# Kernel tuning notes

Hardware: AMD Instinct MI355X
Metric: run time of the kernel (lower is better)

Reference implementation:

```python
import jax, jax.numpy as jnp
import numpy as np

MAX_LEN = 3

def _attention(h, enc, w1, b1, w2):
    # h: [B,H], enc: [B,S,H]
    B, S, H = enc.shape
    hs = jnp.broadcast_to(h[:, None, :], (B, S, H))
    x = jnp.tanh(jnp.concatenate([enc, hs], axis=-1) @ w1.T + b1)  # [B,S,H]
    e = (x @ w2.T)[..., 0]                                         # [B,S]
    alpha = jax.nn.softmax(e, axis=1)
    return jnp.einsum('bs,bsd->bd', alpha, enc)                    # [B,H]

def _gru_cell(x, h, w_ih, w_hh, b_ih, b_hh):
    # torch GRU gate order: r, z, n
    H = h.shape[-1]
    gi = x @ w_ih.T + b_ih   # [B,3H]
    gh = h @ w_hh.T + b_hh
    i_r, i_z, i_n = gi[:, :H], gi[:, H:2*H], gi[:, 2*H:]
    h_r, h_z, h_n = gh[:, :H], gh[:, H:2*H], gh[:, 2*H:]
    r = jax.nn.sigmoid(i_r + h_r)
    z = jax.nn.sigmoid(i_z + h_z)
    n = jnp.tanh(i_n + r * h_n)
    return (1.0 - z) * n + z * h

def setup_inputs() -> dict:
    key = jax.random.key(0)
    ks = jax.random.split(key, 16)
    B, S, H, DW = 1024, 40, 1024, 512
    V0 = V1 = 4000
    EMB_N = V0 + V1 + 1
    sc = lambda fan: 1.0 / np.sqrt(fan)
    inp = {
        'encoder_outputs': jax.random.normal(ks[0], (B, S, H), jnp.float32),
        'encoder_hidden': jax.random.normal(ks[1], (1, B, H), jnp.float32),
        'targets': jax.random.randint(ks[2], (MAX_LEN, B), 0, V0),
        'emb': jax.random.normal(ks[3], (EMB_N, DW), jnp.float32) * 0.02,
        'attn_w1': jax.random.normal(ks[4], (H, 2 * H), jnp.float32) * sc(2 * H),
        'attn_b1': jnp.zeros((H,), jnp.float32),
        'attn_w2': jax.random.normal(ks[5], (1, H), jnp.float32) * sc(H),
        'w_ih': jax.random.normal(ks[6], (3 * H, H + DW), jnp.float32) * sc(H),
        'w_hh': jax.random.normal(ks[7], (3 * H, H), jnp.float32) * sc(H),
        'b_ih': jnp.zeros((3 * H,), jnp.float32),
        'b_hh': jnp.zeros((3 * H,), jnp.float32),
        'out0_w': jax.random.normal(ks[8], (V0, H), jnp.float32) * sc(H),
        'out0_b': jnp.zeros((V0,), jnp.float32),
        'out1_w': jax.random.normal(ks[9], (V1, H), jnp.float32) * sc(H),
        'out1_b': jnp.zeros((V1,), jnp.float32),
    }
    return inp

def reference(encoder_outputs, encoder_hidden, targets, emb, attn_w1, attn_b1,
              attn_w2, w_ih, w_hh, b_ih, b_hh, out0_w, out0_b, out1_w, out1_b):
    B = encoder_outputs.shape[0]
    h = encoder_hidden[0]  # n_layers=1, unidirectional -> init state passthrough
    logs = []
    for t in range(MAX_LEN):
        context = _attention(h, encoder_outputs, attn_w1, attn_b1, attn_w2)
        if t == 0:
            it = jnp.zeros((B,), jnp.int32)
        elif t == 1:
            it = targets[0] + 1
        else:
            it = targets[t - 1] + 36
        x = jnp.concatenate([emb[it], context], axis=1)  # [B, DW+H]
        h = _gru_cell(x, h, w_ih, w_hh, b_ih, b_hh)
        if t == 0 or t == 2:
            logits = h @ out0_w.T + out0_b
        else:
            logits = h @ out1_w.T + out1_b
        logs.append(jax.nn.log_softmax(logits, axis=1))
    return jnp.stack(logs)  # [MAX_LEN, B, V]
```

## Files before the change

kernel.cpp:

```cpp
#include <hip/hip_runtime.h>
#include <hip/hip_bf16.h>
#include <math.h>

#define B_SZ 1024
#define S_SZ 40
#define H_SZ 1024
#define DW_SZ 512
#define V_SZ 4000
#define XW (DW_SZ + H_SZ)
#define NGL 8192

typedef __bf16 bf16x8 __attribute__((ext_vector_type(8)));
typedef float f32x4 __attribute__((ext_vector_type(4)));

__device__ __forceinline__ float fast_tanh(float x) {
    return 1.0f - 2.0f / (1.0f + __expf(2.0f * x));
}
__device__ __forceinline__ float fast_sigmoid(float x) {
    return 1.0f / (1.0f + __expf(-x));
}
__device__ __forceinline__ float bfraw2f(unsigned short u) {
    return __uint_as_float(((unsigned)u) << 16);
}
__device__ __forceinline__ ushort4 cvt4(float4 v) {
    union { ushort4 u; __hip_bfloat16 h[4]; } o;
    o.h[0] = __float2bfloat16(v.x); o.h[1] = __float2bfloat16(v.y);
    o.h[2] = __float2bfloat16(v.z); o.h[3] = __float2bfloat16(v.w);
    return o.u;
}

#define GLL16(gp, lp)                                                                \
    __builtin_amdgcn_global_load_lds((const __attribute__((address_space(1))) void*)(gp), \
                                     (__attribute__((address_space(3))) void*)(lp), 16, 0, 0)

__global__ __launch_bounds__(256, 2) void gemm_bt_pipe128_v1(
    const __hip_bfloat16* __restrict__ A, int lda,
    const __hip_bfloat16* __restrict__ W, int ldw,
    const float* __restrict__ bias,
    __hip_bfloat16* __restrict__ C, int ldc,
    int nbx, int K) {
    extern __shared__ char smem[];
    const int tid = threadIdx.x;
    const int lane = tid & 63;
    const int wave = tid >> 6;
    const int wm = wave >> 1, wn = wave & 1;
    const int fr = lane & 15, fq = lane >> 4;

    int bid = blockIdx.x;
    { const int cpx = gridDim.x >> 3; bid = (bid & 7) * cpx + (bid >> 3); }
    const int by = bid / nbx;
    const int bm = by * 128;
    const int bn = (bid - by * nbx) * 256;

    const int r0 = tid >> 2;
    const int s0 = (tid & 3) ^ ((tid >> 3) & 3);
    const __hip_bfloat16* gA0 = A + (size_t)(bm + r0) * lda + s0 * 8;
    const __hip_bfloat16* gA1 = A + (size_t)(bm + r0 + 64) * lda + s0 * 8;
    const __hip_bfloat16* gW0 = W + (size_t)(bn + r0) * ldw + s0 * 8;
    const __hip_bfloat16* gW1 = W + (size_t)(bn + r0 + 64) * ldw + s0 * 8;
    const __hip_bfloat16* gW2 = W + (size_t)(bn + r0 + 128) * ldw + s0 * 8;
    const __hip_bfloat16* gW3 = W + (size_t)(bn + r0 + 192) * ldw + s0 * 8;
    const int dst0 = tid * 16;

    int aoff[4], boff[8];
#pragma unroll
    for (int mi = 0; mi < 4; ++mi) {
        const int row = wm * 64 + mi * 16 + fr;
        aoff[mi] = row * 64 + ((fq ^ ((row >> 1) & 3)) << 4);
    }
#pragma unroll
    for (int ni = 0; ni < 8; ++ni) {
        const int col = wn * 128 + ni * 16 + fr;
        boff[ni] = 8192 + col * 64 + ((fq ^ ((col >> 1) & 3)) << 4);
    }

    const int NT = K >> 5;
    f32x4 acc[4][8] = {};

#define STAGE_T(t)                                                    \
    do {                                                              \
        char* sb = smem + ((t) % 3) * 24576;                          \
        const int kk = (t) << 5;                                      \
        GLL16(gA0 + kk, sb + dst0);                                   \
        GLL16(gA1 + kk, sb + dst0 + 4096);                            \
        GLL16(gW0 + kk, sb + 8192 + dst0);                            \
        GLL16(gW1 + kk, sb + 8192 + dst0 + 4096);                     \
        GLL16(gW2 + kk, sb + 8192 + dst0 + 8192);                     \
        GLL16(gW3 + kk, sb + 8192 + dst0 + 12288);                    \
    } while (0)

    STAGE_T(0);
    STAGE_T(1);
    __builtin_amdgcn_sched_barrier(0);
    asm volatile("s_waitcnt vmcnt(6)" ::: "memory");
    __builtin_amdgcn_s_barrier();
    __builtin_amdgcn_sched_barrier(0);

    for (int t = 0; t < NT; ++t) {
        const char* sb = smem + (t % 3) * 24576;
        bf16x8 af[4], bg[8];
#pragma unroll
        for (int ni = 0; ni < 8; ++ni) bg[ni] = *reinterpret_cast<const bf16x8*>(sb + boff[ni]);
#pragma unroll
        for (int mi = 0; mi < 4; ++mi) af[mi] = *reinterpret_cast<const bf16x8*>(sb + aoff[mi]);

        if (t + 2 < NT) STAGE_T(t + 2);

        __builtin_amdgcn_s_setprio(1);
#pragma unroll
        for (int mi = 0; mi < 4; ++mi)
#pragma unroll
            for (int ni = 0; ni < 8; ++ni)
                acc[mi][ni] = __builtin_amdgcn_mfma_f32_16x16x32_bf16(af[mi], bg[ni], acc[mi][ni], 0, 0, 0);
        __builtin_amdgcn_s_setprio(0);

        if (t != NT - 1) {
            __builtin_amdgcn_sched_barrier(0);
            if (t + 2 < NT) asm volatile("s_waitcnt vmcnt(6)" ::: "memory");
            else            asm volatile("s_waitcnt vmcnt(0)" ::: "memory");
            __builtin_amdgcn_s_barrier();
            __builtin_amdgcn_sched_barrier(0);
        }
    }
#undef STAGE_T

#pragma unroll
    for (int ni = 0; ni < 8; ++ni) {
        const int col = bn + wn * 128 + ni * 16 + fr;
        const float bb = bias ? bias[col] : 0.0f;
#pragma unroll
        for (int mi = 0; mi < 4; ++mi) {
            const int row0 = bm + wm * 64 + mi * 16 + fq * 4;
#pragma unroll
            for (int r = 0; r < 4; ++r)
                C[(size_t)(row0 + r) * ldc + col] = __float2bfloat16(acc[mi][ni][r] + bb);
        }
    }
}

__global__ __launch_bounds__(512, 2) void gemm_bt_pipe128_v2(
    const __hip_bfloat16* __restrict__ A, int lda,
    const __hip_bfloat16* __restrict__ W, int ldw,
    const float* __restrict__ bias,
    __hip_bfloat16* __restrict__ C, int ldc,
    int nbx, int K) {
    extern __shared__ char smem[];
    const int tid = threadIdx.x;
    const int lane = tid & 63;
    const int wave = tid >> 6;
    const int wm = wave >> 2, wn = wave & 3;
    const int fr = lane & 15, fq = lane >> 4;

    int bid = blockIdx.x;
    { const int cpx = gridDim.x >> 3; bid = (bid & 7) * cpx + (bid >> 3); }
    const int by = bid / nbx;
    const int bm = by * 128;
    const int bn = (bid - by * nbx) * 256;

    const int r0 = tid >> 2;
    const int s0 = (tid & 3) ^ ((tid >> 3) & 3);
    const __hip_bfloat16* gA0 = A + (size_t)(bm + r0) * lda + s0 * 8;
    const __hip_bfloat16* gW0 = W + (size_t)(bn + r0) * ldw + s0 * 8;
    const __hip_bfloat16* gW1 = W + (size_t)(bn + r0 + 128) * ldw + s0 * 8;
    const int dst0 = tid * 16;

    int aoff[4], boff[4];
#pragma unroll
    for (int mi = 0; mi < 4; ++mi) {
        const int row = wm * 64 + mi * 16 + fr;
        aoff[mi] = row * 64 + ((fq ^ ((row >> 1) & 3)) << 4);
    }
#pragma unroll
    for (int ni = 0; ni < 4; ++ni) {
        const int col = wn * 64 + ni * 16 + fr;
        boff[ni] = 8192 + col * 64 + ((fq ^ ((col >> 1) & 3)) << 4);
    }

    const int NT = K >> 5;
    f32x4 acc[4][4] = {};

#define STAGE_T(t)                                                    \
    do {                                                              \
        char* sb = smem + ((t) % 3) * 24576;                          \
        const int kk = (t) << 5;                                      \
        GLL16(gA0 + kk, sb + dst0);                                   \
        GLL16(gW0 + kk, sb + 8192 + dst0);                            \
        GLL16(gW1 + kk, sb + 8192 + dst0 + 8192);                     \
    } while (0)

    STAGE_T(0);
    STAGE_T(1);
    __builtin_amdgcn_sched_barrier(0);
    asm volatile("s_waitcnt vmcnt(3)" ::: "memory");
    __builtin_amdgcn_s_barrier();
    __builtin_amdgcn_sched_barrier(0);

    for (int t = 0; t < NT; ++t) {
        const char* sb = smem + (t % 3) * 24576;
        bf16x8 af[4], bg[4];
#pragma unroll
        for (int ni = 0; ni < 4; ++ni) bg[ni] = *reinterpret_cast<const bf16x8*>(sb + boff[ni]);
#pragma unroll
        for (int mi = 0; mi < 4; ++mi) af[mi] = *reinterpret_cast<const bf16x8*>(sb + aoff[mi]);

        if (t + 2 < NT) STAGE_T(t + 2);

        __builtin_amdgcn_s_setprio(1);
#pragma unroll
        for (int mi = 0; mi < 4; ++mi)
#pragma unroll
            for (int ni = 0; ni < 4; ++ni)
                acc[mi][ni] = __builtin_amdgcn_mfma_f32_16x16x32_bf16(af[mi], bg[ni], acc[mi][ni], 0, 0, 0);
        __builtin_amdgcn_s_setprio(0);

        if (t != NT - 1) {
            __builtin_amdgcn_sched_barrier(0);
            if (t + 2 < NT) asm volatile("s_waitcnt vmcnt(3)" ::: "memory");
            else            asm volatile("s_waitcnt vmcnt(0)" ::: "memory");
            __builtin_amdgcn_s_barrier();
            __builtin_amdgcn_sched_barrier(0);
        }
    }
#undef STAGE_T

#pragma unroll
    for (int ni = 0; ni < 4; ++ni) {
        const int col = bn + wn * 64 + ni * 16 + fr;
        const float bb = bias ? bias[col] : 0.0f;
#pragma unroll
        for (int mi = 0; mi < 4; ++mi) {
            const int row0 = bm + wm * 64 + mi * 16 + fq * 4;
#pragma unroll
            for (int r = 0; r < 4; ++r)
                C[(size_t)(row0 + r) * ldc + col] = __float2bfloat16(acc[mi][ni][r] + bb);
        }
    }
}

#define SB0 0
#define SB1 10240
#define SB2 10496
#define SB3 10752
#define SB4 11520
#define SB5 12672
#define SB6 13672
#define SB7 14672
#define SB8 14696
#define SB9 14720
#define SB10 (14720 + 3072)
#define SB11 (SB10 + 1024)
#define SBTOT (SB11 + 2)
__global__ __launch_bounds__(256) void prep_kernel(
    const float* __restrict__ enc, const float* __restrict__ w1,
    const float* __restrict__ whh, const float* __restrict__ wih,
    const float* __restrict__ o0, const float* __restrict__ o1,
    __hip_bfloat16* __restrict__ enc_bf, __hip_bfloat16* __restrict__ w1a_bf,
    __hip_bfloat16* __restrict__ wall0, __hip_bfloat16* __restrict__ wall1,
    __hip_bfloat16* __restrict__ wih_bf,
    const float* __restrict__ emb, const int* __restrict__ targets,
    __hip_bfloat16* __restrict__ x0, __hip_bfloat16* __restrict__ x1, __hip_bfloat16* __restrict__ x2,
    const float* __restrict__ enc_h, float* __restrict__ h, __hip_bfloat16* __restrict__ h_bf,
    const float* __restrict__ b1, const float* __restrict__ b_hh,
    const float* __restrict__ o0b, const float* __restrict__ o1b,
    float* __restrict__ bias0, float* __restrict__ bias1) {
    const int blk = blockIdx.x;
    const int tid = threadIdx.x;
    ushort4* w0u = reinterpret_cast<ushort4*>(wall0);
    ushort4* w1u = reinterpret_cast<ushort4*>(wall1);

    if (blk < SB1) {
        const int li = blk * 1024 + tid;
        const float4* s = reinterpret_cast<const float4*>(enc);
        float4 v0 = s[li], v1 = s[li + 256], v2 = s[li + 512], v3 = s[li + 768];
        ushort4* d = reinterpret_cast<ushort4*>(enc_bf);
        d[li] = cvt4(v0); d[li + 256] = cvt4(v1); d[li + 512] = cvt4(v2); d[li + 768] = cvt4(v3);
    } else if (blk < SB2) {
        const int r0 = (blk - SB1) * 4;
        const float4* s = reinterpret_cast<const float4*>(w1);
        float4 v0 = s[(r0 + 0) * 512 + tid], v1 = s[(r0 + 1) * 512 + tid],
               v2 = s[(r0 + 2) * 512 + tid], v3 = s[(r0 + 3) * 512 + tid];
        ushort4* d = reinterpret_cast<ushort4*>(w1a_bf);
        const int li = r0 * 256 + tid;
        d[li] = cvt4(v0); d[li + 256] = cvt4(v1); d[li + 512] = cvt4(v2); d[li + 768] = cvt4(v3);
    } else if (blk < SB3) {
        const int r0 = (blk - SB2) * 4;
        const float4* s = reinterpret_cast<const float4*>(w1);
        ushort4 u0 = cvt4(s[(r0 + 0) * 512 + 256 + tid]), u1 = cvt4(s[(r0 + 1) * 512 + 256 + tid]),
                u2 = cvt4(s[(r0 + 2) * 512 + 256 + tid]), u3 = cvt4(s[(r0 + 3) * 512 + 256 + tid]);
        const int li = r0 * 256 + tid;
        w0u[li] = u0; w0u[li + 256] = u1; w0u[li + 512] = u2; w0u[li + 768] = u3;
        w1u[li] = u0; w1u[li + 256] = u1; w1u[li + 512] = u2; w1u[li + 768] = u3;
    } else if (blk < SB4) {
        const int li = (blk - SB3) * 1024 + tid;
        const float4* s = reinterpret_cast<const float4*>(whh);
        ushort4 u0 = cvt4(s[li]), u1 = cvt4(s[li + 256]), u2 = cvt4(s[li + 512]), u3 = cvt4(s[li + 768]);
        w0u[262144 + li] = u0; w0u[262144 + li + 256] = u1;
        w0u[262144 + li + 512] = u2; w0u[262144 + li + 768] = u3;
        w1u[262144 + li] = u0; w1u[262144 + li + 256] = u1;
        w1u[262144 + li + 512] = u2; w1u[262144 + li + 768] = u3;
    } else if (blk < SB5) {
        const int li = (blk - SB4) * 1024 + tid;
        const float4* s = reinterpret_cast<const float4*>(wih);
        float4 v0 = s[li], v1 = s[li + 256], v2 = s[li + 512], v3 = s[li + 768];
        ushort4* d = reinterpret_cast<ushort4*>(wih_bf);
        d[li] = cvt4(v0); d[li + 256] = cvt4(v1); d[li + 512] = cvt4(v2); d[li + 768] = cvt4(v3);
    } else if (blk < SB6) {
        const int li = (blk - SB5) * 1024 + tid;
        const float4* s = reinterpret_cast<const float4*>(o0);
        float4 v0 = s[li], v1 = s[li + 256], v2 = s[li + 512], v3 = s[li + 768];
        w0u[1048576 + li] = cvt4(v0); w0u[1048576 + li + 256] = cvt4(v1);
        w0u[1048576 + li + 512] = cvt4(v2); w0u[1048576 + li + 768] = cvt4(v3);
    } else if (blk < SB7) {
        const int li = (blk - SB6) * 1024 + tid;
        const float4* s = reinterpret_cast<const float4*>(o1);
        float4 v0 = s[li], v1 = s[li + 256], v2 = s[li + 512], v3 = s[li + 768];
        w1u[1048576 + li] = cvt4(v0); w1u[1048576 + li + 256] = cvt4(v1);
        w1u[1048576 + li + 512] = cvt4(v2); w1u[1048576 + li + 768] = cvt4(v3);
    } else if (blk < SB9) {
        const ushort4 z = make_ushort4(0, 0, 0, 0);
        if (blk < SB8) {
            const int li = 2072576 + (blk - SB7) * 1024 + tid;
            w0u[li] = z; w0u[li + 256] = z; w0u[li + 512] = z; w0u[li + 768] = z;
        } else {
            const int li = 2072576 + (blk - SB8) * 1024 + tid;
            w1u[li] = z; w1u[li + 256] = z; w1u[li + 512] = z; w1u[li + 768] = z;
        }
    } else if (blk < SB10) {
        if (tid >= 128) return;
        const int e = blk - SB9;
        const int t = e >> 10;
        const int b = e & 1023;
        int it; __hip_bfloat16* x;
        if (t == 0) { it = 0; x = x0; }
        else if (t == 1) { it = targets[b] + 1; x = x1; }
        else { it = targets[B_SZ + b] + 36; x = x2; }
        float4 v = reinterpret_cast<const float4*>(emb + (size_t)it * DW_SZ)[tid];
        reinterpret_cast<ushort4*>(x + (size_t)b * XW)[tid] = cvt4(v);
    } else if (blk < SB11) {
        const int i = (blk - SB10) * 256 + tid;
        const float4 v = reinterpret_cast<const float4*>(enc_h)[i];
        reinterpret_cast<float4*>(h)[i] = v;
        reinterpret_cast<ushort4*>(h_bf)[i] = cvt4(v);
    } else {
        float* bt = (blk == SB11) ? bias0 : bias1;
        const float* ob = (blk == SB11) ? o0b : o1b;
        for (int j = tid; j < NGL; j += 256) {
            float v;
            if (j < H_SZ) v = b1[j];
            else if (j < 4 * H_SZ) v = b_hh[j - H_SZ];
            else if (j < 4 * H_SZ + V_SZ) v = ob[j - 4 * H_SZ];
            else v = 0.0f;
            bt[j] = v;
        }
    }
}

__global__ __launch_bounds__(256) void attn_ls_kernel(
    const __hip_bfloat16* __restrict__ enc,
    const __hip_bfloat16* __restrict__ enc_proj,
    const __hip_bfloat16* __restrict__ hgl,
    const float* __restrict__ w2,
    __hip_bfloat16* __restrict__ x,
    float* __restrict__ outp,
    int nattn) {
    const int blk = blockIdx.x;
    const int tid = threadIdx.x;
    const int lane = tid & 63, wave = tid >> 6;
    __shared__ float s_e[S_SZ];
    __shared__ float s_red[4];
    __shared__ float s_bc;

    if (blk < nattn) {
        const int b = blk;
        float hp[16], wv[16];
        const unsigned short* hgrow = reinterpret_cast<const unsigned short*>(hgl) + (size_t)b * NGL;
#pragma unroll
        for (int p = 0; p < 4; ++p) {
            const int base = p * 256 + lane * 4;
            ushort4 hu = *reinterpret_cast<const ushort4*>(hgrow + base);
            float4 wq = *reinterpret_cast<const float4*>(w2 + base);
            hp[p * 4 + 0] = bfraw2f(hu.x); hp[p * 4 + 1] = bfraw2f(hu.y);
            hp[p * 4 + 2] = bfraw2f(hu.z); hp[p * 4 + 3] = bfraw2f(hu.w);
            wv[p * 4 + 0] = wq.x; wv[p * 4 + 1] = wq.y;
            wv[p * 4 + 2] = wq.z; wv[p * 4 + 3] = wq.w;
        }

        const unsigned short* ep0 = reinterpret_cast<const unsigned short*>(enc_proj) + (size_t)b * S_SZ * H_SZ;
#pragma unroll 2
        for (int i = 0; i < 10; ++i) {
            const int s = wave + 4 * i;
            const unsigned short* row = ep0 + (size_t)s * H_SZ;
            float acc = 0.f;
#pragma unroll
            for (int p = 0; p < 4; ++p) {
                ushort4 eu = *reinterpret_cast<const ushort4*>(row + p * 256 + lane * 4);
                acc += fast_tanh(bfraw2f(eu.x) + hp[p * 4 + 0]) * wv[p * 4 + 0]
                     + fast_tanh(bfraw2f(eu.y) + hp[p * 4 + 1]) * wv[p * 4 + 1]
                     + fast_tanh(bfraw2f(eu.z) + hp[p * 4 + 2]) * wv[p * 4 + 2]
                     + fast_tanh(bfraw2f(eu.w) + hp[p * 4 + 3]) * wv[p * 4 + 3];
            }
#pragma unroll
            for (int off = 32; off > 0; off >>= 1) acc += __shfl_down(acc, off);
            if (lane == 0) s_e[s] = acc;
        }
        __syncthreads();

        float m = -1e30f;
        for (int s = 0; s < S_SZ; ++s) m = fmaxf(m, s_e[s]);
        float sum = 0.f;
        for (int s = 0; s < S_SZ; ++s) sum += __expf(s_e[s] - m);
        const float inv = 1.0f / sum;

        const ushort4* enc_b = reinterpret_cast<const ushort4*>(enc + (size_t)b * S_SZ * H_SZ);
        float4 acc = make_float4(0.f, 0.f, 0.f, 0.f);
        for (int s = 0; s < S_SZ; ++s) {
            const float a = __expf(s_e[s] - m) * inv;
            ushort4 ev = enc_b[s * 256 + tid];
            acc.x += a * bfraw2f(ev.x); acc.y += a * bfraw2f(ev.y);
            acc.z += a * bfraw2f(ev.z); acc.w += a * bfraw2f(ev.w);
        }
        reinterpret_cast<ushort4*>(x + (size_t)b * XW + DW_SZ)[tid] = cvt4(acc);
    } else {
        const int b = blk - nattn;
        const ushort4* row4 = reinterpret_cast<const ushort4*>(
            reinterpret_cast<const unsigned short*>(hgl) + (size_t)b * NGL + 4096);
        float* orow = outp + (size_t)b * V_SZ;

        float m = -1e30f;
        for (int k = tid; k < V_SZ / 4; k += 256) {
            ushort4 u = row4[k];
            m = fmaxf(m, fmaxf(fmaxf(bfraw2f(u.x), bfraw2f(u.y)), fmaxf(bfraw2f(u.z), bfraw2f(u.w))));
        }
#pragma unroll
        for (int off = 32; off > 0; off >>= 1) m = fmaxf(m, __shfl_down(m, off));
        if (lane == 0) s_red[wave] = m;
        __syncthreads();
        if (tid == 0) s_bc = fmaxf(fmaxf(s_red[0], s_red[1]), fmaxf(s_red[2], s_red[3]));
        __syncthreads();
        m = s_bc;

        float sum = 0.f;
        for (int k = tid; k < V_SZ / 4; k += 256) {
            ushort4 u = row4[k];
            sum += expf(bfraw2f(u.x) - m) + expf(bfraw2f(u.y) - m)
                 + expf(bfraw2f(u.z) - m) + expf(bfraw2f(u.w) - m);
        }
#pragma unroll
        for (int off = 32; off > 0; off >>= 1) sum += __shfl_down(sum, off);
        __syncthreads();
        if (lane == 0) s_red[wave] = sum;
        __syncthreads();
        if (tid == 0) s_bc = logf(s_red[0] + s_red[1] + s_red[2] + s_red[3]) + m;
        __syncthreads();
        const float ls = s_bc;

        for (int k = tid; k < V_SZ / 4; k += 256) {
            ushort4 u = row4[k];
            float4 o = make_float4(bfraw2f(u.x) - ls, bfraw2f(u.y) - ls,
                                   bfraw2f(u.z) - ls, bfraw2f(u.w) - ls);
            reinterpret_cast<float4*>(orow)[k] = o;
        }
    }
}

__global__ __launch_bounds__(256) void gru_gate_kernel(
    const __hip_bfloat16* __restrict__ gi,
    const __hip_bfloat16* __restrict__ hgl,
    float* __restrict__ h,
    __hip_bfloat16* __restrict__ h_bf) {
    const int idx = blockIdx.x * 256 + threadIdx.x;
    const int b = idx >> 10;
    const int j = idx & 1023;
    const unsigned short* gib = reinterpret_cast<const unsigned short*>(gi) + (size_t)b * 3 * H_SZ;
    const unsigned short* ghb = reinterpret_cast<const unsigned short*>(hgl) + (size_t)b * NGL + H_SZ;
    const float i_r = bfraw2f(gib[j]), i_z = bfraw2f(gib[H_SZ + j]), i_n = bfraw2f(gib[2 * H_SZ + j]);
    const float h_r = bfraw2f(ghb[j]), h_z = bfraw2f(ghb[H_SZ + j]), h_n = bfraw2f(ghb[2 * H_SZ + j]);
    const float r = fast_sigmoid(i_r + h_r);
    const float z = fast_sigmoid(i_z + h_z);
    const float n = fast_tanh(i_n + r * h_n);
    const float hv = (1.0f - z) * n + z * h[idx];
    h[idx] = hv;
    h_bf[idx] = __float2bfloat16(hv);
}

extern "C" void kernel_launch(void* const* d_in, const int* in_sizes, int n_in,
                              void* d_out, int out_size, void* d_ws, size_t ws_size,
                              hipStream_t stream) {
    const float* enc    = (const float*)d_in[0];
    const float* enc_h  = (const float*)d_in[1];
    const int*   tgt    = (const int*)d_in[2];
    const float* emb    = (const float*)d_in[3];
    const float* w1     = (const float*)d_in[4];
    const float* b1     = (const float*)d_in[5];
    const float* w2     = (const float*)d_in[6];
    const float* w_ih   = (const float*)d_in[7];
    const float* w_hh   = (const float*)d_in[8];
    const float* b_ih   = (const float*)d_in[9];
    const float* b_hh   = (const float*)d_in[10];
    const float* out0_w = (const float*)d_in[11];
    const float* out0_b = (const float*)d_in[12];
    const float* out1_w = (const float*)d_in[13];
    const float* out1_b = (const float*)d_in[14];
    float* out = (float*)d_out;

    char* wp = (char*)d_ws;
    auto carve = [&](size_t bytes) { char* p = wp; wp += (bytes + 255) & ~(size_t)255; return p; };
    __hip_bfloat16* enc_bf  = (__hip_bfloat16*)carve((size_t)B_SZ * S_SZ * H_SZ * 2);
    __hip_bfloat16* encp_bf = (__hip_bfloat16*)carve((size_t)B_SZ * S_SZ * H_SZ * 2);
    __hip_bfloat16* w1a_bf  = (__hip_bfloat16*)carve((size_t)H_SZ * H_SZ * 2);
    __hip_bfloat16* wall0   = (__hip_bfloat16*)carve((size_t)NGL * H_SZ * 2);
    __hip_bfloat16* wall1   = (__hip_bfloat16*)carve((size_t)NGL * H_SZ * 2);
    __hip_bfloat16* wih_bf  = (__hip_bfloat16*)carve((size_t)3 * H_SZ * XW * 2);
    float*          bias0   = (float*)carve((size_t)NGL * 4);
    float*          bias1   = (float*)carve((size_t)NGL * 4);
    float*          h       = (float*)carve((size_t)B_SZ * H_SZ * 4);
    __hip_bfloat16* h_bf    = (__hip_bfloat16*)carve((size_t)B_SZ * H_SZ * 2);
    __hip_bfloat16* hgl     = (__hip_bfloat16*)carve((size_t)B_SZ * NGL * 2);
    __hip_bfloat16* x_bf[3];
    for (int t = 0; t < 3; ++t) x_bf[t] = (__hip_bfloat16*)carve((size_t)B_SZ * XW * 2);
    __hip_bfloat16* gi_bf   = (__hip_bfloat16*)carve((size_t)B_SZ * 3 * H_SZ * 2);

    prep_kernel<<<SBTOT, 256, 0, stream>>>(enc, w1, w_hh, w_ih, out0_w, out1_w,
                                           enc_bf, w1a_bf, wall0, wall1, wih_bf,
                                           emb, tgt, x_bf[0], x_bf[1], x_bf[2],
                                           enc_h, h, h_bf, b1, b_hh, out0_b, out1_b,
                                           bias0, bias1);

    gemm_bt_pipe128_v1<<<(B_SZ * S_SZ / 128) * (H_SZ / 256), 256, 3 * 24576, stream>>>(
        enc_bf, H_SZ, w1a_bf, H_SZ, nullptr, encp_bf, H_SZ, H_SZ / 256, H_SZ);

    gemm_bt_pipe128_v2<<<(B_SZ / 128) * 16, 512, 3 * 24576, stream>>>(
        h_bf, H_SZ, wall0, H_SZ, bias0, hgl, NGL, 16, H_SZ);

    attn_ls_kernel<<<B_SZ, 256, 0, stream>>>(enc_bf, encp_bf, hgl, w2, x_bf[0], out, B_SZ);

    for (int t = 0; t < 3; ++t) {
        gemm_bt_pipe128_v2<<<(B_SZ / 128) * 12, 512, 3 * 24576, stream>>>(
            x_bf[t], XW, wih_bf, XW, b_ih, gi_bf, 3 * H_SZ, 12, XW);

        gru_gate_kernel<<<(B_SZ * H_SZ) / 256, 256, 0, stream>>>(gi_bf, hgl, h, h_bf);

        if (t == 0) {
            gemm_bt_pipe128_v2<<<(B_SZ / 128) * 32, 512, 3 * 24576, stream>>>(
                h_bf, H_SZ, wall0, H_SZ, bias0, hgl, NGL, 32, H_SZ);
        } else if (t == 1) {
            gemm_bt_pipe128_v2<<<(B_SZ / 128) * 32, 512, 3 * 24576, stream>>>(
                h_bf, H_SZ, wall1, H_SZ, bias1, hgl, NGL, 32, H_SZ);
        } else {
            gemm_bt_pipe128_v2<<<(B_SZ / 128) * 16, 512, 3 * 24576, stream>>>(
                h_bf, H_SZ, wall0 + (size_t)4 * H_SZ * H_SZ, H_SZ, bias0 + 4 * H_SZ,
                hgl + 4 * H_SZ, NGL, 16, H_SZ);
        }

        float* outp = out + (size_t)t * B_SZ * V_SZ;
        if (t < 2) {
            attn_ls_kernel<<<2 * B_SZ, 256, 0, stream>>>(enc_bf, encp_bf, hgl, w2, x_bf[t + 1],
                                                         outp, B_SZ);
        } else {
            attn_ls_kernel<<<B_SZ, 256, 0, stream>>>(enc_bf, encp_bf, hgl, w2, x_bf[0],
                                                     outp, 0);
        }
    }
}
```

Measured before the change: 490.0 us.

## Overlap weight casts with encoder projection GEMM via tail blocks

Splits the prep kernel so that only the inputs the encoder-projection GEMM needs are cast up front. The remaining weight casts (W1 hidden half, W_hh, W_ih, output weights and zero padding) run as extra tail blocks of the GEMM launch, so their memory traffic can overlap with GEMM compute. The enc cast also moves to 8-wide packed bf16 stores. The cost is that the cast blocks reserve the GEMM's large dynamic shared memory allocation, which may limit how many of them fit per CU, and the blocks interleave in scheduling.

```diff
diff --git a/kernel.cpp b/kernel.cpp
--- a/kernel.cpp
+++ b/kernel.cpp
@@ -12,6 +12,7 @@
 
 typedef __bf16 bf16x8 __attribute__((ext_vector_type(8)));
 typedef float f32x4 __attribute__((ext_vector_type(4)));
+typedef unsigned short u16x8 __attribute__((ext_vector_type(8)));
 
 __device__ __forceinline__ float fast_tanh(float x) {
     return 1.0f - 2.0f / (1.0f + __expf(2.0f * x));
@@ -28,26 +29,96 @@
     o.h[2] = __float2bfloat16(v.z); o.h[3] = __float2bfloat16(v.w);
     return o.u;
 }
+__device__ __forceinline__ u16x8 pack8(float4 a, float4 b) {
+    union { u16x8 v; ushort4 h[2]; } o;
+    o.h[0] = cvt4(a); o.h[1] = cvt4(b);
+    return o.v;
+}
 
 #define GLL16(gp, lp)                                                                \
     __builtin_amdgcn_global_load_lds((const __attribute__((address_space(1))) void*)(gp), \
                                      (__attribute__((address_space(3))) void*)(lp), 16, 0, 0)
 
-__global__ __launch_bounds__(256, 2) void gemm_bt_pipe128_v1(
+__device__ void cast_tail_block(int blk, int tid,
+                                const float* __restrict__ w1, const float* __restrict__ whh,
+                                const float* __restrict__ wih, const float* __restrict__ o0,
+                                const float* __restrict__ o1,
+                                __hip_bfloat16* __restrict__ wall0,
+                                __hip_bfloat16* __restrict__ wall1,
+                                __hip_bfloat16* __restrict__ wih_bf) {
+    ushort4* w0u = reinterpret_cast<ushort4*>(wall0);
+    ushort4* w1u = reinterpret_cast<ushort4*>(wall1);
+    if (blk < 256) {
+        const int r0 = blk * 4;
+        const float4* s = reinterpret_cast<const float4*>(w1);
+        ushort4 u0 = cvt4(s[(r0 + 0) * 512 + 256 + tid]), u1 = cvt4(s[(r0 + 1) * 512 + 256 + tid]),
+                u2 = cvt4(s[(r0 + 2) * 512 + 256 + tid]), u3 = cvt4(s[(r0 + 3) * 512 + 256 + tid]);
+        const int li = r0 * 256 + tid;
+        w0u[li] = u0; w0u[li + 256] = u1; w0u[li + 512] = u2; w0u[li + 768] = u3;
+        w1u[li] = u0; w1u[li + 256] = u1; w1u[li + 512] = u2; w1u[li + 768] = u3;
+    } else if (blk < 1024) {
+        const int li = (blk - 256) * 1024 + tid;
+        const float4* s = reinterpret_cast<const float4*>(whh);
+        ushort4 u0 = cvt4(s[li]), u1 = cvt4(s[li + 256]), u2 = cvt4(s[li + 512]), u3 = cvt4(s[li + 768]);
+        w0u[262144 + li] = u0; w0u[262144 + li + 256] = u1;
+        w0u[262144 + li + 512] = u2; w0u[262144 + li + 768] = u3;
+        w1u[262144 + li] = u0; w1u[262144 + li + 256] = u1;
+        w1u[262144 + li + 512] = u2; w1u[262144 + li + 768] = u3;
+    } else if (blk < 2176) {
+        const int li = (blk - 1024) * 1024 + tid;
+        const float4* s = reinterpret_cast<const float4*>(wih);
+        float4 v0 = s[li], v1 = s[li + 256], v2 = s[li + 512], v3 = s[li + 768];
+        ushort4* d = reinterpret_cast<ushort4*>(wih_bf);
+        d[li] = cvt4(v0); d[li + 256] = cvt4(v1); d[li + 512] = cvt4(v2); d[li + 768] = cvt4(v3);
+    } else if (blk < 3176) {
+        const int li = (blk - 2176) * 1024 + tid;
+        const float4* s = reinterpret_cast<const float4*>(o0);
+        float4 v0 = s[li], v1 = s[li + 256], v2 = s[li + 512], v3 = s[li + 768];
+        w0u[1048576 + li] = cvt4(v0); w0u[1048576 + li + 256] = cvt4(v1);
+        w0u[1048576 + li + 512] = cvt4(v2); w0u[1048576 + li + 768] = cvt4(v3);
+    } else if (blk < 4176) {
+        const int li = (blk - 3176) * 1024 + tid;
+        const float4* s = reinterpret_cast<const float4*>(o1);
+        float4 v0 = s[li], v1 = s[li + 256], v2 = s[li + 512], v3 = s[li + 768];
+        w1u[1048576 + li] = cvt4(v0); w1u[1048576 + li + 256] = cvt4(v1);
+        w1u[1048576 + li + 512] = cvt4(v2); w1u[1048576 + li + 768] = cvt4(v3);
+    } else {
+        const ushort4 z = make_ushort4(0, 0, 0, 0);
+        if (blk < 4200) {
+            const int li = 2072576 + (blk - 4176) * 1024 + tid;
+            w0u[li] = z; w0u[li + 256] = z; w0u[li + 512] = z; w0u[li + 768] = z;
+        } else {
+            const int li = 2072576 + (blk - 4200) * 1024 + tid;
+            w1u[li] = z; w1u[li + 256] = z; w1u[li + 512] = z; w1u[li + 768] = z;
+        }
+    }
+}
+
+__global__ __launch_bounds__(256, 2) void gemm_enc_cast(
     const __hip_bfloat16* __restrict__ A, int lda,
     const __hip_bfloat16* __restrict__ W, int ldw,
-    const float* __restrict__ bias,
     __hip_bfloat16* __restrict__ C, int ldc,
-    int nbx, int K) {
+    int nbx, int K, int gemm_nb,
+    const float* __restrict__ w1, const float* __restrict__ whh,
+    const float* __restrict__ wih, const float* __restrict__ o0,
+    const float* __restrict__ o1,
+    __hip_bfloat16* __restrict__ wall0, __hip_bfloat16* __restrict__ wall1,
+    __hip_bfloat16* __restrict__ wih_bf) {
     extern __shared__ char smem[];
     const int tid = threadIdx.x;
+
+    if ((int)blockIdx.x >= gemm_nb) {
+        cast_tail_block(blockIdx.x - gemm_nb, tid, w1, whh, wih, o0, o1, wall0, wall1, wih_bf);
+        return;
+    }
+
     const int lane = tid & 63;
     const int wave = tid >> 6;
     const int wm = wave >> 1, wn = wave & 1;
     const int fr = lane & 15, fq = lane >> 4;
 
     int bid = blockIdx.x;
-    { const int cpx = gridDim.x >> 3; bid = (bid & 7) * cpx + (bid >> 3); }
+    { const int cpx = gemm_nb >> 3; bid = (bid & 7) * cpx + (bid >> 3); }
     const int by = bid / nbx;
     const int bm = by * 128;
     const int bn = (bid - by * nbx) * 256;
@@ -127,13 +198,12 @@
 #pragma unroll
     for (int ni = 0; ni < 8; ++ni) {
         const int col = bn + wn * 128 + ni * 16 + fr;
-        const float bb = bias ? bias[col] : 0.0f;
 #pragma unroll
         for (int mi = 0; mi < 4; ++mi) {
             const int row0 = bm + wm * 64 + mi * 16 + fq * 4;
 #pragma unroll
             for (int r = 0; r < 4; ++r)
-                C[(size_t)(row0 + r) * ldc + col] = __float2bfloat16(acc[mi][ni][r] + bb);
+                C[(size_t)(row0 + r) * ldc + col] = __float2bfloat16(acc[mi][ni][r]);
         }
     }
 }
@@ -237,26 +307,14 @@
     }
 }
 
-#define SB0 0
-#define SB1 10240
-#define SB2 10496
-#define SB3 10752
-#define SB4 11520
-#define SB5 12672
-#define SB6 13672
-#define SB7 14672
-#define SB8 14696
-#define SB9 14720
-#define SB10 (14720 + 3072)
-#define SB11 (SB10 + 1024)
-#define SBTOT (SB11 + 2)
-__global__ __launch_bounds__(256) void prep_kernel(
+#define PA_ENC 10240
+#define PA_W1A (PA_ENC + 256)
+#define PA_EMB (PA_W1A + 3072)
+#define PA_H   (PA_EMB + 1024)
+#define PA_TOT (PA_H + 2)
+__global__ __launch_bounds__(256) void prep_a_kernel(
     const float* __restrict__ enc, const float* __restrict__ w1,
-    const float* __restrict__ whh, const float* __restrict__ wih,
-    const float* __restrict__ o0, const float* __restrict__ o1,
     __hip_bfloat16* __restrict__ enc_bf, __hip_bfloat16* __restrict__ w1a_bf,
-    __hip_bfloat16* __restrict__ wall0, __hip_bfloat16* __restrict__ wall1,
-    __hip_bfloat16* __restrict__ wih_bf,
     const float* __restrict__ emb, const int* __restrict__ targets,
     __hip_bfloat16* __restrict__ x0, __hip_bfloat16* __restrict__ x1, __hip_bfloat16* __restrict__ x2,
     const float* __restrict__ enc_h, float* __restrict__ h, __hip_bfloat16* __restrict__ h_bf,
@@ -265,69 +323,27 @@
     float* __restrict__ bias0, float* __restrict__ bias1) {
     const int blk = blockIdx.x;
     const int tid = threadIdx.x;
-    ushort4* w0u = reinterpret_cast<ushort4*>(wall0);
-    ushort4* w1u = reinterpret_cast<ushort4*>(wall1);
-
-    if (blk < SB1) {
-        const int li = blk * 1024 + tid;
+
+    if (blk < PA_ENC) {
         const float4* s = reinterpret_cast<const float4*>(enc);
-        float4 v0 = s[li], v1 = s[li + 256], v2 = s[li + 512], v3 = s[li + 768];
-        ushort4* d = reinterpret_cast<ushort4*>(enc_bf);
-        d[li] = cvt4(v0); d[li + 256] = cvt4(v1); d[li + 512] = cvt4(v2); d[li + 768] = cvt4(v3);
-    } else if (blk < SB2) {
-        const int r0 = (blk - SB1) * 4;
+        u16x8* d = reinterpret_cast<u16x8*>(enc_bf);
+        const int f0 = blk * 1024 + tid * 2;
+        const int f1 = f0 + 512;
+        float4 a0 = s[f0], a1 = s[f0 + 1];
+        float4 b0 = s[f1], b1v = s[f1 + 1];
+        d[blk * 512 + tid] = pack8(a0, a1);
+        d[blk * 512 + 256 + tid] = pack8(b0, b1v);
+    } else if (blk < PA_W1A) {
+        const int r0 = (blk - PA_ENC) * 4;
         const float4* s = reinterpret_cast<const float4*>(w1);
         float4 v0 = s[(r0 + 0) * 512 + tid], v1 = s[(r0 + 1) * 512 + tid],
                v2 = s[(r0 + 2) * 512 + tid], v3 = s[(r0 + 3) * 512 + tid];
         ushort4* d = reinterpret_cast<ushort4*>(w1a_bf);
         const int li = r0 * 256 + tid;
         d[li] = cvt4(v0); d[li + 256] = cvt4(v1); d[li + 512] = cvt4(v2); d[li + 768] = cvt4(v3);
-    } else if (blk < SB3) {
-        const int r0 = (blk - SB2) * 4;
-        const float4* s = reinterpret_cast<const float4*>(w1);
-        ushort4 u0 = cvt4(s[(r0 + 0) * 512 + 256 + tid]), u1 = cvt4(s[(r0 + 1) * 512 + 256 + tid]),
-                u2 = cvt4(s[(r0 + 2) * 512 + 256 + tid]), u3 = cvt4(s[(r0 + 3) * 512 + 256 + tid]);
-        const int li = r0 * 256 + tid;
-        w0u[li] = u0; w0u[li + 256] = u1; w0u[li + 512] = u2; w0u[li + 768] = u3;
-        w1u[li] = u0; w1u[li + 256] = u1; w1u[li + 512] = u2; w1u[li + 768] = u3;
-    } else if (blk < SB4) {
-        const int li = (blk - SB3) * 1024 + tid;
-        const float4* s = reinterpret_cast<const float4*>(whh);
-        ushort4 u0 = cvt4(s[li]), u1 = cvt4(s[li + 256]), u2 = cvt4(s[li + 512]), u3 = cvt4(s[li + 768]);
-        w0u[262144 + li] = u0; w0u[262144 + li + 256] = u1;
-        w0u[262144 + li + 512] = u2; w0u[262144 + li + 768] = u3;
-        w1u[262144 + li] = u0; w1u[262144 + li + 256] = u1;
-        w1u[262144 + li + 512] = u2; w1u[262144 + li + 768] = u3;
-    } else if (blk < SB5) {
-        const int li = (blk - SB4) * 1024 + tid;
-        const float4* s = reinterpret_cast<const float4*>(wih);
-        float4 v0 = s[li], v1 = s[li + 256], v2 = s[li + 512], v3 = s[li + 768];
-        ushort4* d = reinterpret_cast<ushort4*>(wih_bf);
-        d[li] = cvt4(v0); d[li + 256] = cvt4(v1); d[li + 512] = cvt4(v2); d[li + 768] = cvt4(v3);
-    } else if (blk < SB6) {
-        const int li = (blk - SB5) * 1024 + tid;
-        const float4* s = reinterpret_cast<const float4*>(o0);
-        float4 v0 = s[li], v1 = s[li + 256], v2 = s[li + 512], v3 = s[li + 768];
-        w0u[1048576 + li] = cvt4(v0); w0u[1048576 + li + 256] = cvt4(v1);
-        w0u[1048576 + li + 512] = cvt4(v2); w0u[1048576 + li + 768] = cvt4(v3);
-    } else if (blk < SB7) {
-        const int li = (blk - SB6) * 1024 + tid;
-        const float4* s = reinterpret_cast<const float4*>(o1);
-        float4 v0 = s[li], v1 = s[li + 256], v2 = s[li + 512], v3 = s[li + 768];
-        w1u[1048576 + li] = cvt4(v0); w1u[1048576 + li + 256] = cvt4(v1);
-        w1u[1048576 + li + 512] = cvt4(v2); w1u[1048576 + li + 768] = cvt4(v3);
-    } else if (blk < SB9) {
-        const ushort4 z = make_ushort4(0, 0, 0, 0);
-        if (blk < SB8) {
-            const int li = 2072576 + (blk - SB7) * 1024 + tid;
-            w0u[li] = z; w0u[li + 256] = z; w0u[li + 512] = z; w0u[li + 768] = z;
-        } else {
-            const int li = 2072576 + (blk - SB8) * 1024 + tid;
-            w1u[li] = z; w1u[li + 256] = z; w1u[li + 512] = z; w1u[li + 768] = z;
-        }
-    } else if (blk < SB10) {
+    } else if (blk < PA_EMB) {
         if (tid >= 128) return;
-        const int e = blk - SB9;
+        const int e = blk - PA_W1A;
         const int t = e >> 10;
         const int b = e & 1023;
         int it; __hip_bfloat16* x;
@@ -336,14 +352,14 @@
         else { it = targets[B_SZ + b] + 36; x = x2; }
         float4 v = reinterpret_cast<const float4*>(emb + (size_t)it * DW_SZ)[tid];
         reinterpret_cast<ushort4*>(x + (size_t)b * XW)[tid] = cvt4(v);
-    } else if (blk < SB11) {
-        const int i = (blk - SB10) * 256 + tid;
+    } else if (blk < PA_H) {
+        const int i = (blk - PA_EMB) * 256 + tid;
         const float4 v = reinterpret_cast<const float4*>(enc_h)[i];
         reinterpret_cast<float4*>(h)[i] = v;
         reinterpret_cast<ushort4*>(h_bf)[i] = cvt4(v);
     } else {
-        float* bt = (blk == SB11) ? bias0 : bias1;
-        const float* ob = (blk == SB11) ? o0b : o1b;
+        float* bt = (blk == PA_H) ? bias0 : bias1;
+        const float* ob = (blk == PA_H) ? o0b : o1b;
         for (int j = tid; j < NGL; j += 256) {
             float v;
             if (j < H_SZ) v = b1[j];
@@ -520,14 +536,15 @@
     for (int t = 0; t < 3; ++t) x_bf[t] = (__hip_bfloat16*)carve((size_t)B_SZ * XW * 2);
     __hip_bfloat16* gi_bf   = (__hip_bfloat16*)carve((size_t)B_SZ * 3 * H_SZ * 2);
 
-    prep_kernel<<<SBTOT, 256, 0, stream>>>(enc, w1, w_hh, w_ih, out0_w, out1_w,
-                                           enc_bf, w1a_bf, wall0, wall1, wih_bf,
-                                           emb, tgt, x_bf[0], x_bf[1], x_bf[2],
-                                           enc_h, h, h_bf, b1, b_hh, out0_b, out1_b,
-                                           bias0, bias1);
-
-    gemm_bt_pipe128_v1<<<(B_SZ * S_SZ / 128) * (H_SZ / 256), 256, 3 * 24576, stream>>>(
-        enc_bf, H_SZ, w1a_bf, H_SZ, nullptr, encp_bf, H_SZ, H_SZ / 256, H_SZ);
+    prep_a_kernel<<<PA_TOT, 256, 0, stream>>>(enc, w1, enc_bf, w1a_bf,
+                                              emb, tgt, x_bf[0], x_bf[1], x_bf[2],
+                                              enc_h, h, h_bf, b1, b_hh, out0_b, out1_b,
+                                              bias0, bias1);
+
+    const int gemm_nb = (B_SZ * S_SZ / 128) * (H_SZ / 256);
+    gemm_enc_cast<<<gemm_nb + 4224, 256, 3 * 24576, stream>>>(
+        enc_bf, H_SZ, w1a_bf, H_SZ, encp_bf, H_SZ, H_SZ / 256, H_SZ, gemm_nb,
+        w1, w_hh, w_ih, out0_w, out1_w, wall0, wall1, wih_bf);
 
     gemm_bt_pipe128_v2<<<(B_SZ / 128) * 16, 512, 3 * 24576, stream>>>(
         h_bf, H_SZ, wall0, H_SZ, bias0, hgl, NGL, 16, H_SZ);
```

Result: faster. 479.7 us (median of 2 runs) (-2.1%).
